# Optimization experiments

Measured on AMD Instinct MI355X. Metric: run time of the kernel, lower is better.

## Reference

```python
import jax, jax.numpy as jnp
import numpy as np

N_NODES = 50000
N_EDGES = 1600000
N_GRAPHS = 512
IN_DIM = 384
HID = 128


def gcn_conv(x, W, b, src, dst, n_nodes):
    # PyG GCNConv: h = W^T x, then propagate with sym norm over A + I (self-loops).
    h = x @ W  # [N, out]
    # self-loops
    loop = jnp.arange(n_nodes, dtype=src.dtype)
    s = jnp.concatenate([src, loop])
    d = jnp.concatenate([dst, loop])
    ones = jnp.ones(s.shape[0], dtype=h.dtype)
    deg = jax.ops.segment_sum(ones, d, num_segments=n_nodes)  # in-degree incl self-loop
    dis = jnp.where(deg > 0, jax.lax.rsqrt(deg), 0.0)
    norm = dis[s] * dis[d]  # [E+N]
    msg = h[s] * norm[:, None]  # gather + scale
    out = jax.ops.segment_sum(msg, d, num_segments=n_nodes)  # scatter-add
    return out + b


def global_mean_pool(x, batch, num_graphs):
    sums = jax.ops.segment_sum(x, batch, num_segments=num_graphs)
    cnt = jax.ops.segment_sum(jnp.ones(x.shape[0], dtype=x.dtype), batch, num_segments=num_graphs)
    return sums / jnp.maximum(cnt, 1.0)[:, None]


def setup_inputs() -> dict:
    key = jax.random.key(0)
    ks = jax.random.split(key, 12)
    x = jax.random.normal(ks[0], (N_NODES, IN_DIM), dtype=jnp.float32)
    edge_index = jax.random.randint(ks[1], (2, N_EDGES), 0, N_NODES, dtype=jnp.int64 if jax.config.jax_enable_x64 else jnp.int32)
    batch = jnp.sort(jax.random.randint(ks[2], (N_NODES,), 0, N_GRAPHS, dtype=jnp.int32))
    def glorot(k, shape):
        lim = float(np.sqrt(6.0 / (shape[0] + shape[1])))
        return jax.random.uniform(k, shape, jnp.float32, -lim, lim)
    return {
        "x": x,
        "edge_index": edge_index,
        "batch": batch,
        "W1": glorot(ks[3], (IN_DIM, HID)),
        "b1": jnp.zeros((HID,), jnp.float32),
        "W2": glorot(ks[4], (HID, HID)),
        "b2": jnp.zeros((HID,), jnp.float32),
        "Wl1": glorot(ks[5], (HID, HID // 2)),
        "bl1": jnp.zeros((HID // 2,), jnp.float32),
        "Wl2": glorot(ks[6], (HID // 2, 5)),
        "bl2": jnp.zeros((5,), jnp.float32),
    }


def reference(x, edge_index, batch, W1, b1, W2, b2, Wl1, bl1, Wl2, bl2):
    src, dst = edge_index[0], edge_index[1]
    n = x.shape[0]
    h = jax.nn.relu(gcn_conv(x, W1, b1, src, dst, n))
    h = jax.nn.relu(gcn_conv(h, W2, b2, src, dst, n))
    g = global_mean_pool(h, batch, N_GRAPHS)  # [G, HID]
    g = jax.nn.relu(g @ Wl1 + bl1)
    return jax.nn.sigmoid(g @ Wl2 + bl2)  # [G, 5]
```

## Files before the change

### kernel.cpp

```cpp
#include <hip/hip_runtime.h>
#include <hip/hip_bf16.h>

#define HID 128
#define NGRAPH 512
#define IN_DIM 384

__device__ __forceinline__ float bf2f(unsigned int u16) {
    union { float f; unsigned int i; } x;
    x.i = u16 << 16;
    return x.f;
}
__device__ __forceinline__ unsigned short f2bf(float f) {
    union { float f; unsigned int i; } x;
    x.f = f;
    unsigned int r = (x.i + 0x7FFFu + ((x.i >> 16) & 1u)) >> 16;
    return (unsigned short)r;
}

__global__ void deg_kernel(const int* __restrict__ dst, int* __restrict__ deg, int E) {
    int e = blockIdx.x * blockDim.x + threadIdx.x;
    if (e < E) atomicAdd(&deg[dst[e]], 1);
}

__global__ void dis_kernel(const int* __restrict__ deg, float* __restrict__ dis, int n) {
    int v = blockIdx.x * blockDim.x + threadIdx.x;
    if (v < n) dis[v] = rsqrtf((float)(deg[v] + 1));
}

__global__ __launch_bounds__(256) void scan_part(const int* __restrict__ deg, int* __restrict__ row,
                                                 int* __restrict__ blockSums, int n) {
    __shared__ int ts[256];
    const int b = blockIdx.x, t = threadIdx.x;
    const int base = b * 1024 + t * 4;
    int v0 = (base + 0 < n) ? deg[base + 0] : 0;
    int v1 = (base + 1 < n) ? deg[base + 1] : 0;
    int v2 = (base + 2 < n) ? deg[base + 2] : 0;
    int v3 = (base + 3 < n) ? deg[base + 3] : 0;
    const int s = v0 + v1 + v2 + v3;
    ts[t] = s;
    __syncthreads();
    for (int off = 1; off < 256; off <<= 1) {
        int x = (t >= off) ? ts[t - off] : 0;
        __syncthreads();
        ts[t] += x;
        __syncthreads();
    }
    int p = ts[t] - s;
    if (base + 0 < n) { row[base + 0] = p; p += v0; }
    if (base + 1 < n) { row[base + 1] = p; p += v1; }
    if (base + 2 < n) { row[base + 2] = p; p += v2; }
    if (base + 3 < n) { row[base + 3] = p; }
    if (t == 255) blockSums[b] = ts[255];
}

__global__ void scan_tops(int* __restrict__ blockSums, int nb) {
    if (threadIdx.x == 0 && blockIdx.x == 0) {
        int acc = 0;
        for (int i = 0; i < nb; i++) { int v = blockSums[i]; blockSums[i] = acc; acc += v; }
    }
}

__global__ __launch_bounds__(256) void scan_add(int* __restrict__ row, int* __restrict__ cursor,
                                                const int* __restrict__ blockSums, int n, int E) {
    const int b = blockIdx.x, t = threadIdx.x;
    const int off = blockSums[b];
    const int base = b * 1024 + t * 4;
#pragma unroll
    for (int j = 0; j < 4; j++) {
        int i = base + j;
        if (i < n) { int v = row[i] + off; row[i] = v; cursor[i] = v; }
    }
    if (b == 0 && t == 0) row[n] = E;
}

__global__ void fill_kernel(const int* __restrict__ src, const int* __restrict__ dst,
                            int* __restrict__ cursor, int* __restrict__ csr_src, int E) {
    int e = blockIdx.x * blockDim.x + threadIdx.x;
    if (e < E) {
        int pos = atomicAdd(&cursor[dst[e]], 1);
        csr_src[pos] = src[e];
    }
}

template <int K>
__global__ __launch_bounds__(256) void gemm_tile(const float* __restrict__ X,
                                                 const float* __restrict__ W,
                                                 const float* __restrict__ dis,
                                                 unsigned short* __restrict__ outb, int n) {
    constexpr int KC = 32;
    __shared__ float asT[KC][68];
    __shared__ float bs[KC * HID];
    const int t = threadIdx.x;
    const int tx = t & 31;
    const int ty = t >> 5;
    const int row0 = blockIdx.x * 64;

    float4 acc[8];
#pragma unroll
    for (int j = 0; j < 8; j++) acc[j] = make_float4(0.f, 0.f, 0.f, 0.f);

    const int ar = t >> 3;
    const int af = t & 7;

    for (int k0 = 0; k0 < K; k0 += KC) {
#pragma unroll
        for (int half = 0; half < 2; half++) {
            const int r = ar + half * 32;
            const int gr = row0 + r;
            float4 a = make_float4(0.f, 0.f, 0.f, 0.f);
            if (gr < n) a = *(const float4*)&X[(long)gr * K + k0 + af * 4];
            asT[af * 4 + 0][r] = a.x;
            asT[af * 4 + 1][r] = a.y;
            asT[af * 4 + 2][r] = a.z;
            asT[af * 4 + 3][r] = a.w;
        }
        {
            const float4* wp = (const float4*)&W[(long)k0 * HID];
            float4* bp = (float4*)bs;
#pragma unroll
            for (int i = 0; i < 4; i++) bp[t + i * 256] = wp[t + i * 256];
        }
        __syncthreads();
#pragma unroll 8
        for (int kk = 0; kk < KC; kk++) {
            const float4 a0 = *(const float4*)&asT[kk][ty * 8];
            const float4 a1 = *(const float4*)&asT[kk][ty * 8 + 4];
            const float4 b  = *(const float4*)&bs[kk * HID + tx * 4];
            acc[0].x = fmaf(a0.x, b.x, acc[0].x); acc[0].y = fmaf(a0.x, b.y, acc[0].y);
            acc[0].z = fmaf(a0.x, b.z, acc[0].z); acc[0].w = fmaf(a0.x, b.w, acc[0].w);
            acc[1].x = fmaf(a0.y, b.x, acc[1].x); acc[1].y = fmaf(a0.y, b.y, acc[1].y);
            acc[1].z = fmaf(a0.y, b.z, acc[1].z); acc[1].w = fmaf(a0.y, b.w, acc[1].w);
            acc[2].x = fmaf(a0.z, b.x, acc[2].x); acc[2].y = fmaf(a0.z, b.y, acc[2].y);
            acc[2].z = fmaf(a0.z, b.z, acc[2].z); acc[2].w = fmaf(a0.z, b.w, acc[2].w);
            acc[3].x = fmaf(a0.w, b.x, acc[3].x); acc[3].y = fmaf(a0.w, b.y, acc[3].y);
            acc[3].z = fmaf(a0.w, b.z, acc[3].z); acc[3].w = fmaf(a0.w, b.w, acc[3].w);
            acc[4].x = fmaf(a1.x, b.x, acc[4].x); acc[4].y = fmaf(a1.x, b.y, acc[4].y);
            acc[4].z = fmaf(a1.x, b.z, acc[4].z); acc[4].w = fmaf(a1.x, b.w, acc[4].w);
            acc[5].x = fmaf(a1.y, b.x, acc[5].x); acc[5].y = fmaf(a1.y, b.y, acc[5].y);
            acc[5].z = fmaf(a1.y, b.z, acc[5].z); acc[5].w = fmaf(a1.y, b.w, acc[5].w);
            acc[6].x = fmaf(a1.z, b.x, acc[6].x); acc[6].y = fmaf(a1.z, b.y, acc[6].y);
            acc[6].z = fmaf(a1.z, b.z, acc[6].z); acc[6].w = fmaf(a1.z, b.w, acc[6].w);
            acc[7].x = fmaf(a1.w, b.x, acc[7].x); acc[7].y = fmaf(a1.w, b.y, acc[7].y);
            acc[7].z = fmaf(a1.w, b.z, acc[7].z); acc[7].w = fmaf(a1.w, b.w, acc[7].w);
        }
        __syncthreads();
    }

#pragma unroll
    for (int j = 0; j < 8; j++) {
        const int v = row0 + ty * 8 + j;
        if (v < n) {
            const float dv = dis[v];
            ushort4 r;
            r.x = f2bf(acc[j].x * dv);
            r.y = f2bf(acc[j].y * dv);
            r.z = f2bf(acc[j].z * dv);
            r.w = f2bf(acc[j].w * dv);
            *(ushort4*)&outb[(long)v * HID + tx * 4] = r;
        }
    }
}

template <bool POOL>
__global__ __launch_bounds__(256) void agg_kernel(const unsigned short* __restrict__ hsb,
                                                  const int* __restrict__ csr_src,
                                                  const int* __restrict__ row,
                                                  const float* __restrict__ dis,
                                                  const float* __restrict__ bias,
                                                  const int* __restrict__ batch,
                                                  float* __restrict__ out,
                                                  float* __restrict__ sums,
                                                  int* __restrict__ cnt, int n) {
    const int v = blockIdx.x * 4 + (threadIdx.x >> 6);
    if (v >= n) return;
    const int lane = threadIdx.x & 63;
    const int c = lane << 1;

    const int rs = row[v];
    const int re = row[v + 1];
    float ax0 = 0.f, ay0 = 0.f, ax1 = 0.f, ay1 = 0.f;

    for (int base = rs; base < re; base += 64) {
        int m = re - base;
        if (m > 64) m = 64;
        const int idx = (base + lane < re) ? csr_src[base + lane] : 0;
        int j = 0;
        for (; j + 4 <= m; j += 4) {
            const int s0 = __shfl(idx, j);
            const int s1 = __shfl(idx, j + 1);
            const int s2 = __shfl(idx, j + 2);
            const int s3 = __shfl(idx, j + 3);
            const unsigned int m0 = *(const unsigned int*)&hsb[(long)s0 * HID + c];
            const unsigned int m1 = *(const unsigned int*)&hsb[(long)s1 * HID + c];
            const unsigned int m2 = *(const unsigned int*)&hsb[(long)s2 * HID + c];
            const unsigned int m3 = *(const unsigned int*)&hsb[(long)s3 * HID + c];
            ax0 += bf2f(m0 & 0xffffu); ay0 += bf2f(m0 >> 16);
            ax1 += bf2f(m1 & 0xffffu); ay1 += bf2f(m1 >> 16);
            ax0 += bf2f(m2 & 0xffffu); ay0 += bf2f(m2 >> 16);
            ax1 += bf2f(m3 & 0xffffu); ay1 += bf2f(m3 >> 16);
        }
        for (; j < m; j++) {
            const int s = __shfl(idx, j);
            const unsigned int mm = *(const unsigned int*)&hsb[(long)s * HID + c];
            ax0 += bf2f(mm & 0xffffu); ay0 += bf2f(mm >> 16);
        }
    }

    const unsigned int selfm = *(const unsigned int*)&hsb[(long)v * HID + c];
    const float sx = ax0 + ax1 + bf2f(selfm & 0xffffu);
    const float sy = ay0 + ay1 + bf2f(selfm >> 16);
    const float dv = dis[v];
    const float rx = fmaxf(fmaf(dv, sx, bias[c]), 0.f);
    const float ry = fmaxf(fmaf(dv, sy, bias[c + 1]), 0.f);
    if (POOL) {
        const int g = batch[v];
        unsafeAtomicAdd(&sums[g * HID + c], rx);
        unsafeAtomicAdd(&sums[g * HID + c + 1], ry);
        if (lane == 0) atomicAdd(&cnt[g], 1);
    } else {
        float2 r; r.x = rx; r.y = ry;
        *(float2*)&out[(long)v * HID + c] = r;
    }
}

__global__ __launch_bounds__(64) void mlp_kernel(const float* __restrict__ sums,
                                                 const int* __restrict__ cnt,
                                                 const float* __restrict__ Wl1,
                                                 const float* __restrict__ bl1,
                                                 const float* __restrict__ Wl2,
                                                 const float* __restrict__ bl2,
                                                 float* __restrict__ out) {
    const int g = blockIdx.x, t = threadIdx.x;
    __shared__ float mean[HID];
    __shared__ float hid[64];
    const float c = fmaxf((float)cnt[g], 1.0f);
    mean[t] = sums[g * HID + t] / c;
    mean[t + 64] = sums[g * HID + 64 + t] / c;
    __syncthreads();
    float acc = bl1[t];
#pragma unroll 4
    for (int k = 0; k < HID; k++) acc = fmaf(mean[k], Wl1[k * 64 + t], acc);
    hid[t] = fmaxf(acc, 0.f);
    __syncthreads();
    if (t < 5) {
        float a = bl2[t];
#pragma unroll 4
        for (int k = 0; k < 64; k++) a = fmaf(hid[k], Wl2[k * 5 + t], a);
        out[g * 5 + t] = 1.f / (1.f + expf(-a));
    }
}

extern "C" void kernel_launch(void* const* d_in, const int* in_sizes, int n_in,
                              void* d_out, int out_size, void* d_ws, size_t ws_size,
                              hipStream_t stream) {
    const float* x   = (const float*)d_in[0];
    const int* ei    = (const int*)d_in[1];
    const int* batch = (const int*)d_in[2];
    const float* W1  = (const float*)d_in[3];
    const float* b1  = (const float*)d_in[4];
    const float* W2  = (const float*)d_in[5];
    const float* b2  = (const float*)d_in[6];
    const float* Wl1 = (const float*)d_in[7];
    const float* bl1 = (const float*)d_in[8];
    const float* Wl2 = (const float*)d_in[9];
    const float* bl2 = (const float*)d_in[10];
    float* out = (float*)d_out;

    const int n = in_sizes[0] / IN_DIM;
    const int E = in_sizes[1] / 2;
    const int* src = ei;
    const int* dst = ei + E;

    char* ws = (char*)d_ws;
    size_t off = 0;
    auto alloc = [&](size_t bytes) {
        void* p = ws + off;
        off = (off + bytes + 255) & ~(size_t)255;
        return p;
    };
    int*   deg       = (int*)alloc((size_t)n * 4);
    float* dis       = (float*)alloc((size_t)n * 4);
    int*   row       = (int*)alloc((size_t)(n + 1) * 4);
    int*   cursor    = (int*)alloc((size_t)n * 4);
    int*   csr_src   = (int*)alloc((size_t)E * 4);
    int*   blockSums = (int*)alloc(256 * 4);
    unsigned short* hsb = (unsigned short*)alloc((size_t)n * HID * 2);
    float* buf1 = (float*)alloc((size_t)n * HID * 4);
    float* sums = (float*)alloc((size_t)NGRAPH * HID * 4);
    int*   cnt  = (int*)alloc((size_t)NGRAPH * 4);
    (void)ws_size;

    const int nb = (n + 1023) / 1024;
    const int gemmBlocks = (n + 63) / 64;
    const int aggBlocks  = (n + 3) / 4;

    hipMemsetAsync(deg, 0, (size_t)n * 4, stream);
    deg_kernel<<<(E + 255) / 256, 256, 0, stream>>>(dst, deg, E);
    dis_kernel<<<(n + 255) / 256, 256, 0, stream>>>(deg, dis, n);
    scan_part<<<nb, 256, 0, stream>>>(deg, row, blockSums, n);
    scan_tops<<<1, 64, 0, stream>>>(blockSums, nb);
    scan_add<<<nb, 256, 0, stream>>>(row, cursor, blockSums, n, E);
    fill_kernel<<<(E + 255) / 256, 256, 0, stream>>>(src, dst, cursor, csr_src, E);

    gemm_tile<IN_DIM><<<gemmBlocks, 256, 0, stream>>>(x, W1, dis, hsb, n);
    agg_kernel<false><<<aggBlocks, 256, 0, stream>>>(hsb, csr_src, row, dis, b1, batch,
                                                     buf1, nullptr, nullptr, n);

    gemm_tile<HID><<<gemmBlocks, 256, 0, stream>>>(buf1, W2, dis, hsb, n);
    hipMemsetAsync(sums, 0, (size_t)NGRAPH * HID * 4, stream);
    hipMemsetAsync(cnt, 0, (size_t)NGRAPH * 4, stream);
    agg_kernel<true><<<aggBlocks, 256, 0, stream>>>(hsb, csr_src, row, dis, b2, batch,
                                                    nullptr, sums, cnt, n);

    mlp_kernel<<<NGRAPH, 64, 0, stream>>>(sums, cnt, Wl1, bl1, Wl2, bl2, out);
}
```

Before: 635.4 us.

## Split wavefront into four edge groups with 16-byte row gathers in aggregation

The aggregation kernel now splits each 64-lane wavefront into four 16-lane subgroups. Each subgroup handles a different edge and loads a full 256-byte bf16 row with uint4 loads. Up to 8 loads per lane are issued before any accumulation, to raise memory-level parallelism. Partial sums are combined across subgroups with xor shuffles. The cost is more registers, a per-lane csr_src load for every edge instead of a broadcast shuffle, and an extra cross-lane reduction.

```diff
diff --git a/kernel.cpp b/kernel.cpp
--- a/kernel.cpp
+++ b/kernel.cpp
@@ -174,52 +174,65 @@
     const int v = blockIdx.x * 4 + (threadIdx.x >> 6);
     if (v >= n) return;
     const int lane = threadIdx.x & 63;
-    const int c = lane << 1;
+    const int sub = lane >> 4;
+    const int lc  = lane & 15;
 
     const int rs = row[v];
     const int re = row[v + 1];
-    float ax0 = 0.f, ay0 = 0.f, ax1 = 0.f, ay1 = 0.f;
-
-    for (int base = rs; base < re; base += 64) {
-        int m = re - base;
-        if (m > 64) m = 64;
-        const int idx = (base + lane < re) ? csr_src[base + lane] : 0;
-        int j = 0;
-        for (; j + 4 <= m; j += 4) {
-            const int s0 = __shfl(idx, j);
-            const int s1 = __shfl(idx, j + 1);
-            const int s2 = __shfl(idx, j + 2);
-            const int s3 = __shfl(idx, j + 3);
-            const unsigned int m0 = *(const unsigned int*)&hsb[(long)s0 * HID + c];
-            const unsigned int m1 = *(const unsigned int*)&hsb[(long)s1 * HID + c];
-            const unsigned int m2 = *(const unsigned int*)&hsb[(long)s2 * HID + c];
-            const unsigned int m3 = *(const unsigned int*)&hsb[(long)s3 * HID + c];
-            ax0 += bf2f(m0 & 0xffffu); ay0 += bf2f(m0 >> 16);
-            ax1 += bf2f(m1 & 0xffffu); ay1 += bf2f(m1 >> 16);
-            ax0 += bf2f(m2 & 0xffffu); ay0 += bf2f(m2 >> 16);
-            ax1 += bf2f(m3 & 0xffffu); ay1 += bf2f(m3 >> 16);
-        }
-        for (; j < m; j++) {
-            const int s = __shfl(idx, j);
-            const unsigned int mm = *(const unsigned int*)&hsb[(long)s * HID + c];
-            ax0 += bf2f(mm & 0xffffu); ay0 += bf2f(mm >> 16);
-        }
-    }
-
-    const unsigned int selfm = *(const unsigned int*)&hsb[(long)v * HID + c];
-    const float sx = ax0 + ax1 + bf2f(selfm & 0xffffu);
-    const float sy = ay0 + ay1 + bf2f(selfm >> 16);
+
+    float acc[8];
+#pragma unroll
+    for (int i = 0; i < 8; i++) acc[i] = 0.f;
+
+    for (int base = rs; base < re; base += 32) {
+        uint4 w[8];
+        int vld[8];
+#pragma unroll
+        for (int p = 0; p < 8; p++) {
+            const int pe = base + p * 4;
+            if (pe < re) {
+                const int ei = pe + sub;
+                const int idx = csr_src[(ei < re) ? ei : (re - 1)];
+                w[p] = *(const uint4*)&hsb[(long)idx * HID + (lc << 3)];
+                vld[p] = (ei < re);
+            } else {
+                w[p] = make_uint4(0u, 0u, 0u, 0u);
+                vld[p] = 0;
+            }
+        }
+#pragma unroll
+        for (int p = 0; p < 8; p++) {
+            if (vld[p]) {
+                const uint4 ww = w[p];
+                acc[0] += bf2f(ww.x & 0xffffu); acc[1] += bf2f(ww.x >> 16);
+                acc[2] += bf2f(ww.y & 0xffffu); acc[3] += bf2f(ww.y >> 16);
+                acc[4] += bf2f(ww.z & 0xffffu); acc[5] += bf2f(ww.z >> 16);
+                acc[6] += bf2f(ww.w & 0xffffu); acc[7] += bf2f(ww.w >> 16);
+            }
+        }
+    }
+
+#pragma unroll
+    for (int i = 0; i < 8; i++) {
+        acc[i] += __shfl_xor(acc[i], 16, 64);
+        acc[i] += __shfl_xor(acc[i], 32, 64);
+    }
+
+    const int col = (lc << 3) + (sub << 1);
+    const unsigned int selfm = *(const unsigned int*)&hsb[(long)v * HID + col];
+    const float sx = acc[(sub << 1) + 0] + bf2f(selfm & 0xffffu);
+    const float sy = acc[(sub << 1) + 1] + bf2f(selfm >> 16);
     const float dv = dis[v];
-    const float rx = fmaxf(fmaf(dv, sx, bias[c]), 0.f);
-    const float ry = fmaxf(fmaf(dv, sy, bias[c + 1]), 0.f);
+    const float rx = fmaxf(fmaf(dv, sx, bias[col]), 0.f);
+    const float ry = fmaxf(fmaf(dv, sy, bias[col + 1]), 0.f);
     if (POOL) {
         const int g = batch[v];
-        unsafeAtomicAdd(&sums[g * HID + c], rx);
-        unsafeAtomicAdd(&sums[g * HID + c + 1], ry);
+        unsafeAtomicAdd(&sums[g * HID + col], rx);
+        unsafeAtomicAdd(&sums[g * HID + col + 1], ry);
         if (lane == 0) atomicAdd(&cnt[g], 1);
     } else {
         float2 r; r.x = rx; r.y = ry;
-        *(float2*)&out[(long)v * HID + c] = r;
+        *(float2*)&out[(long)v * HID + col] = r;
     }
 }
 
```

Measured after the change: 658.0 us. 1.04x slower.
